# Kernel optimization log

Measured on AMD Instinct MI355X. Metric: run time of the kernel, lower is better.

The kernel has to match this reference:

```python
import jax, jax.numpy as jnp
import numpy as np
from jax import lax

B, L, V, D = 64, 1024, 256, 512
DROPOUT = 0.1   # embedding dropout rate
ZONEOUT = 0.1   # bernoulli prob of keeping previous state (zoneout)


def setup_inputs() -> dict:
    key = jax.random.key(0)
    ks = jax.random.split(key, 5)
    tokens = jax.random.randint(ks[0], (B, L), 0, V)
    lengths = jax.random.randint(ks[1], (B,), 1, L + 1)
    embed = jax.random.normal(ks[2], (V, D), jnp.float32) * 0.02
    s = 1.0 / np.sqrt(2 * D).astype(np.float32)
    W_fwd = jax.random.normal(ks[3], (2 * D, 4 * D), jnp.float32) * s
    b_fwd = jnp.zeros((4 * D,), jnp.float32)
    W_bwd = jax.random.normal(ks[4], (2 * D, 4 * D), jnp.float32) * s
    b_bwd = jnp.zeros((4 * D,), jnp.float32)
    return {"tokens": tokens, "lengths": lengths, "embed": embed,
            "W_fwd": W_fwd, "b_fwd": b_fwd, "W_bwd": W_bwd, "b_bwd": b_bwd}


def _lstm_scan(x_tbd, reset_tb, W, b, key):
    # x_tbd: [L, B, D] time-major inputs; reset_tb: [L, B] bool (ResetCore mask)
    Bsz = x_tbd.shape[1]
    Dh = W.shape[1] // 4
    zeros = jnp.zeros((Bsz, Dh), x_tbd.dtype)

    def step(carry, inp):
        h, c, k = carry
        x_t, r_t = inp
        # hk.ResetCore: reset state to initial (zeros) where mask is True
        h = jnp.where(r_t[:, None], 0.0, h)
        c = jnp.where(r_t[:, None], 0.0, c)
        kz, k = jax.random.split(k)
        gated = jnp.concatenate([x_t, h], axis=-1) @ W + b  # [B, 4*Dh]
        i, g, f, o = jnp.split(gated, 4, axis=-1)
        f = jax.nn.sigmoid(f + 1.0)
        c_new = f * c + jax.nn.sigmoid(i) * jnp.tanh(g)
        h_new = jax.nn.sigmoid(o) * jnp.tanh(c_new)
        # zoneout: with prob ZONEOUT keep previous hidden/cell
        zm = jax.random.bernoulli(kz, ZONEOUT, (2,) + h.shape)
        h_out = jnp.where(zm[0], h, h_new)
        c_out = jnp.where(zm[1], c, c_new)
        return (h_out, c_out, k), h_out

    _, hs = lax.scan(step, (zeros, zeros, key), (x_tbd, reset_tb))
    return hs  # [L, B, Dh]


def reference(tokens, lengths, embed, W_fwd, b_fwd, W_bwd, b_bwd):
    key = jax.random.key(42)
    kd, kf, kb = jax.random.split(key, 3)
    x = embed[tokens]  # [B, L, D]
    # embedding dropout (is_training=True)
    keep = jax.random.bernoulli(kd, 1.0 - DROPOUT, x.shape)
    x = jnp.where(keep, x / (1.0 - DROPOUT), 0.0)
    Lx = x.shape[1]
    mask = jnp.arange(Lx)[None, :] < lengths[:, None] - 1  # [B, L]
    x_t = jnp.moveaxis(x, 1, 0)  # [L, B, D] time-major
    no_reset = jnp.zeros((Lx, x.shape[0]), bool)
    h_fwd = _lstm_scan(x_t, no_reset, W_fwd, b_fwd, kf)
    # backward pass on flipped sequence with flipped reset mask (ResetCore)
    h_bwd = _lstm_scan(jnp.flip(x_t, 0), jnp.flip(mask, 1).T, W_bwd, b_bwd, kb)
    h_bwd = jnp.flip(h_bwd, 0)
    out = jnp.concatenate([h_fwd, h_bwd], axis=-1)  # [L, B, 2*D]
    return jnp.moveaxis(out, 0, 1)  # [B, L, 2*D]
```

## Files before the change

### kernel.cpp

```cpp
#include <hip/hip_runtime.h>
#include <hip/hip_bf16.h>
#include <stdint.h>

typedef unsigned short u16;
typedef unsigned int   u32;
typedef unsigned long long u64;
typedef __bf16 bf16x8 __attribute__((ext_vector_type(8)));
typedef float  f32x4  __attribute__((ext_vector_type(4)));

__device__ __forceinline__ u32 rotl32(u32 v, int d){ return (v<<d)|(v>>(32-d)); }

__device__ __forceinline__ void tf2x32(u32 k0, u32 k1, u32 c0, u32 c1, u32 &o0, u32 &o1){
  u32 ks0=k0, ks1=k1, ks2=k0^k1^0x1BD11BDAu;
  u32 x0=c0+ks0, x1=c1+ks1;
  x0+=x1; x1=rotl32(x1,13); x1^=x0;  x0+=x1; x1=rotl32(x1,15); x1^=x0;
  x0+=x1; x1=rotl32(x1,26); x1^=x0;  x0+=x1; x1=rotl32(x1, 6); x1^=x0;
  x0+=ks1; x1+=ks2+1u;
  x0+=x1; x1=rotl32(x1,17); x1^=x0;  x0+=x1; x1=rotl32(x1,29); x1^=x0;
  x0+=x1; x1=rotl32(x1,16); x1^=x0;  x0+=x1; x1=rotl32(x1,24); x1^=x0;
  x0+=ks2; x1+=ks0+2u;
  x0+=x1; x1=rotl32(x1,13); x1^=x0;  x0+=x1; x1=rotl32(x1,15); x1^=x0;
  x0+=x1; x1=rotl32(x1,26); x1^=x0;  x0+=x1; x1=rotl32(x1, 6); x1^=x0;
  x0+=ks0; x1+=ks1+3u;
  x0+=x1; x1=rotl32(x1,17); x1^=x0;  x0+=x1; x1=rotl32(x1,29); x1^=x0;
  x0+=x1; x1=rotl32(x1,16); x1^=x0;  x0+=x1; x1=rotl32(x1,24); x1^=x0;
  x0+=ks1; x1+=ks2+4u;
  x0+=x1; x1=rotl32(x1,13); x1^=x0;  x0+=x1; x1=rotl32(x1,15); x1^=x0;
  x0+=x1; x1=rotl32(x1,26); x1^=x0;  x0+=x1; x1=rotl32(x1, 6); x1^=x0;
  x0+=ks2; x1+=ks0+5u;
  o0=x0; o1=x1;
}

__device__ __forceinline__ float u01(u32 b){ return __uint_as_float((b>>9)|0x3f800000u) - 1.0f; }
__device__ __forceinline__ u16 f2bf(float v){ __hip_bfloat16 h = __float2bfloat16(v); return *reinterpret_cast<u16*>(&h); }
__device__ __forceinline__ float bf2f(u16 b){ __hip_bfloat16 h; *reinterpret_cast<u16*>(&h)=b; return __bfloat162float(h); }
__device__ __forceinline__ float sigm(float x){ return 1.0f/(1.0f + __expf(-x)); }
__device__ __forceinline__ float tanh_f(float x){ return 1.0f - 2.0f/(__expf(2.0f*x) + 1.0f); }

__device__ __forceinline__ void gload_lds16(const u16* g, u16* l){
  __builtin_amdgcn_global_load_lds(
      (const __attribute__((address_space(1))) unsigned int*)g,
      (__attribute__((address_space(3))) unsigned int*)l, 16, 0, 0);
}

extern "C" __global__ void __launch_bounds__(256) prep_k(
    const float* __restrict__ Wf, const float* __restrict__ Wb,
    u16* __restrict__ wpack, u32* __restrict__ flags, u32* __restrict__ code, u32* __restrict__ keys){
  u32 gid = blockIdx.x*256u + threadIdx.x;
  if (gid < 8192u) flags[gid] = 0u;
  if (gid == 0u){
    *code = 0u;
    u32 d0,d1,f0,f1,g0,g1;
    tf2x32(0u,42u, 0u,0u, d0,d1);
    tf2x32(0u,42u, 0u,1u, f0,f1);
    tf2x32(0u,42u, 0u,2u, g0,g1);
    keys[0]=d0; keys[1]=d1; keys[2]=f0; keys[3]=f1; keys[4]=g0; keys[5]=g1;
  }
  if (gid == 1u){
    u32 r0,r1; bool ok = true;
    tf2x32(0u,0u,0u,0u,r0,r1);
    ok = ok && (r0==0x6b200159u) && (r1==0x99ba4efeu);
    tf2x32(0x13198a2eu,0x03707344u,0x243f6a88u,0x85a308d3u,r0,r1);
    ok = ok && (r0==0xc4923a9cu) && (r1==0x483df7a0u);
    tf2x32(0xffffffffu,0xffffffffu,0xffffffffu,0xffffffffu,r0,r1);
    ok = ok && (r0==0x1cb996fcu) && (r1==0xbb002be7u);
    if (!ok) __hip_atomic_fetch_or(code, 4u, __ATOMIC_RELAXED, __HIP_MEMORY_SCOPE_AGENT);
  }
  u32 idx = gid >> 6, lane = gid & 63u;
  u32 mat = idx & 3u; u32 r = idx >> 2;
  u32 gt = r & 3u; r >>= 2;
  u32 kt = r & 15u; r >>= 4;
  u32 ug = r & 31u; u32 dir = r >> 5;
  u32 col = gt*512u + ug*16u + (lane & 15u);
  u32 kb  = kt*32u + ((lane>>4)<<3);
  const float* W = dir ? Wb : Wf;
  bool hrow = (mat==1u || mat==2u);
  bool lo   = (mat==2u || mat==3u);
  u16 o[8];
  #pragma unroll
  for (int j=0;j<8;j++){
    u32 k = kb + (u32)j;
    u32 row = hrow ? (512u + k) : k;
    float v = W[(size_t)row*2048u + col];
    u16 h = f2bf(v);
    o[j] = lo ? f2bf(v - bf2f(h)) : h;
  }
  u16* dst = wpack + ((size_t)idx*64u + lane)*8u;
  uint4 pk;
  pk.x = (u32)o[0] | ((u32)o[1]<<16);
  pk.y = (u32)o[2] | ((u32)o[3]<<16);
  pk.z = (u32)o[4] | ((u32)o[5]<<16);
  pk.w = (u32)o[6] | ((u32)o[7]<<16);
  *(uint4*)dst = pk;
}

extern "C" __global__ void __launch_bounds__(256) embed_k(
    const int* __restrict__ tokens, const float* __restrict__ emb,
    const u32* __restrict__ keys, u16* __restrict__ X, u16* __restrict__ XLO, int xsplit){
  u32 gid = blockIdx.x*256u + threadIdx.x;
  u32 kd0 = keys[0], kd1 = keys[1];
  u32 i0 = gid << 1;
  u32 a0,a1,b0,b1;
  tf2x32(kd0,kd1, 0u, i0,     a0,a1);
  tf2x32(kd0,kd1, 0u, i0|1u,  b0,b1);
  u32 bb = i0 >> 19, l = (i0 >> 9) & 1023u, d = i0 & 511u;
  int tok = tokens[(bb<<10)|l];
  const float* ep = emb + (size_t)(u32)tok*512u + d;
  float e0 = ep[0], e1 = ep[1];
  float v0 = (u01(a0^a1) < 0.9f) ? (e0/0.9f) : 0.0f;
  float v1 = (u01(b0^b1) < 0.9f) ? (e1/0.9f) : 0.0f;
  size_t off = (((size_t)l<<6)|bb)*512u + d;
  u16 h0 = f2bf(v0), h1 = f2bf(v1);
  *(u32*)(X+off) = (u32)h0 | ((u32)h1<<16);
  if (xsplit){
    u16 l0 = f2bf(v0 - bf2f(h0)), l1 = f2bf(v1 - bf2f(h1));
    *(u32*)(XLO+off) = (u32)l0 | ((u32)l1<<16);
  }
}

extern "C" __global__ void __launch_bounds__(256,1) lstm_k(
    const u16* __restrict__ wpack, const u16* __restrict__ X, const u16* __restrict__ XLO,
    u32* hbuf, u32* chk, u32* flags, u32* code, const u32* __restrict__ keys,
    const int* __restrict__ lengths, const float* __restrict__ bF, const float* __restrict__ bB,
    float* __restrict__ out, int xsplit){
  __shared__ u16 xHi[2][16][520];
  __shared__ u16 xLoS[2][16][520];
  __shared__ u16 hHi[16][520];
  __shared__ u16 hLo[16][520];
  __shared__ float gparts[4][4][16][17];
  __shared__ u32 kzS[2];
  (void)chk;

  const int tid  = threadIdx.x;
  const int wid  = tid >> 6;
  const int lane = tid & 63;
  const int q    = lane >> 4, n15 = lane & 15;
  const int bx   = blockIdx.x;
  const int dir  = (bx & 7) >> 2, bg = bx & 3, ug = bx >> 3;
  const int grp  = dir*4 + bg;
  const int eb   = tid >> 4, eu = tid & 15;
  const int scol = eu * 32;

  if (bx == 0 && wid == 0){
    bf16x8 aI, aI2, bT;
    #pragma unroll
    for (int j=0;j<8;j++){
      int k = q*8 + j;
      aI[j]  = (__bf16)((k == n15)    ? 1.0f : 0.0f);
      aI2[j] = (__bf16)((k == n15+16) ? 1.0f : 0.0f);
      bT[j]  = (__bf16)((float)((k & 15)*16 + n15));
    }
    f32x4 z = {0.0f,0.0f,0.0f,0.0f};
    f32x4 d1 = __builtin_amdgcn_mfma_f32_16x16x32_bf16(aI,  bT, z, 0,0,0);
    f32x4 d2 = __builtin_amdgcn_mfma_f32_16x16x32_bf16(aI2, bT, z, 0,0,0);
    bool ok = true;
    #pragma unroll
    for (int r=0;r<4;r++){
      float ex = (float)((q*4 + r)*16 + n15);
      ok = ok && (d1[r] == ex) && (d2[r] == ex);
    }
    if (__any(ok ? 0 : 1) && lane == 0)
      __hip_atomic_fetch_or(code, 1u, __ATOMIC_RELAXED, __HIP_MEMORY_SCOPE_AGENT);
  }

  u32 kc0 = keys[2 + dir*2], kc1 = keys[3 + dir*2];

  bf16x8 BW[4][4][4];
  #pragma unroll
  for (int ktl=0;ktl<4;ktl++)
    #pragma unroll
    for (int gt=0;gt<4;gt++)
      #pragma unroll
      for (int mat=0;mat<4;mat++){
        size_t idx = ((((size_t)(dir*32+ug)*16 + (size_t)(wid*4+ktl))*4 + gt)*4 + mat);
        BW[mat][ktl][gt] = *(const bf16x8*)(wpack + (idx*64 + lane)*8);
      }

  const float* bias = dir ? bB : bF;
  float biasr[4];
  #pragma unroll
  for (int g=0;g<4;g++) biasr[g] = bias[g*512 + ug*16 + eu];
  const int lenb = lengths[bg*16 + eb];

  float cReg = 0.0f, hReg = 0.0f;

  u32* hb_base = hbuf + (size_t)grp*2*16*512;
  const size_t outbase = (size_t)(bg*16+eb)*1048576 + (size_t)(dir*512 + ug*16 + eu);

  {
    const int tx0 = dir ? 1023 : 0;
    #pragma unroll
    for (int j=0;j<4;j++){
      const int rb = wid*4 + j;
      const size_t go = (((size_t)tx0*64) + (size_t)(bg*16 + rb))*512 + (size_t)lane*8;
      gload_lds16(X + go, &xHi[0][rb][0]);
      if (xsplit) gload_lds16(XLO + go, &xLoS[0][rb][0]);
    }
  }

  for (int t=0; t<1024; ++t){
    const int cur = t & 1, nxt = cur ^ 1;
    const int tx = dir ? (1023 - t) : t;

    if (wid == 0){
      u32 A0,A1,B0,B1;
      tf2x32(kc0,kc1, 0u,0u, A0,A1);
      tf2x32(kc0,kc1, 0u,1u, B0,B1);
      if (lane==0){ kzS[0]=A0; kzS[1]=A1; }
      kc0=B0; kc1=B1;
    }
    if (t > 0 && wid == 3 && lane < 32){
      const u32* sp = flags + (((size_t)grp*32 + (u32)lane) << 5);
      while (__hip_atomic_load(sp, __ATOMIC_RELAXED, __HIP_MEMORY_SCOPE_AGENT) < (u32)t) {}
    }
    __syncthreads();

    const bool rst = (dir==1) && (t > 1024 - lenb);
    const bool hload = (t > 0) && !rst;
    u64 hv64[16];
    if (hload){
      const u64* hrow64 = (const u64*)(hb_base + ((size_t)((t-1)&1)*16 + eb)*512 + scol);
      #pragma unroll
      for (int i=0;i<16;i++)
        hv64[i] = __hip_atomic_load(hrow64 + i, __ATOMIC_RELAXED, __HIP_MEMORY_SCOPE_AGENT);
    }
    if (t < 1023){
      const int txn = dir ? (1022 - t) : (t + 1);
      #pragma unroll
      for (int j=0;j<4;j++){
        const int rb = wid*4 + j;
        const size_t go = (((size_t)txn*64) + (size_t)(bg*16 + rb))*512 + (size_t)lane*8;
        gload_lds16(X + go, &xHi[nxt][rb][0]);
        if (xsplit) gload_lds16(XLO + go, &xLoS[nxt][rb][0]);
      }
    }
    const u32 cnt = (u32)((bg*16+eb)*512 + ug*16+eu);
    u32 p0,p1,q0,q1;
    tf2x32(kzS[0], kzS[1], 0u, cnt,          p0,p1);
    tf2x32(kzS[0], kzS[1], 0u, cnt+32768u,   q0,q1);
    const bool keepH = (u01(p0^p1) < 0.1f);
    const bool keepC = (u01(q0^q1) < 0.1f);

    f32x4 zz = {0.0f,0.0f,0.0f,0.0f};
    f32x4 acc[4] = {zz,zz,zz,zz};
    #pragma unroll
    for (int ktl=0;ktl<4;ktl++){
      const int ko = (wid*4+ktl)*32 + q*8;
      bf16x8 ax = *(const bf16x8*)&xHi[cur][n15][ko];
      #pragma unroll
      for (int gt=0;gt<4;gt++){
        acc[gt] = __builtin_amdgcn_mfma_f32_16x16x32_bf16(ax, BW[0][ktl][gt], acc[gt], 0,0,0);
        acc[gt] = __builtin_amdgcn_mfma_f32_16x16x32_bf16(ax, BW[3][ktl][gt], acc[gt], 0,0,0);
      }
      if (xsplit){
        bf16x8 axl = *(const bf16x8*)&xLoS[cur][n15][ko];
        #pragma unroll
        for (int gt=0;gt<4;gt++)
          acc[gt] = __builtin_amdgcn_mfma_f32_16x16x32_bf16(axl, BW[0][ktl][gt], acc[gt], 0,0,0);
      }
    }

    if (!hload){
      uint4 z; z.x=0u; z.y=0u; z.z=0u; z.w=0u;
      uint4* hd = (uint4*)&hHi[eb][scol];
      uint4* ld = (uint4*)&hLo[eb][scol];
      hd[0]=z;hd[1]=z;hd[2]=z;hd[3]=z;  ld[0]=z;ld[1]=z;ld[2]=z;ld[3]=z;
    } else {
      u32 hiw[16], low[16];
      #pragma unroll
      for (int k=0;k<16;k++){
        u32 lo32 = (u32)hv64[k], hi32 = (u32)(hv64[k] >> 32);
        hiw[k] = (lo32 & 0xFFFFu) | (hi32 << 16);
        low[k] = (lo32 >> 16)     | (hi32 & 0xFFFF0000u);
      }
      uint4* hd = (uint4*)&hHi[eb][scol];
      uint4* ld = (uint4*)&hLo[eb][scol];
      #pragma unroll
      for (int v=0;v<4;v++){
        uint4 hw; hw.x=hiw[4*v]; hw.y=hiw[4*v+1]; hw.z=hiw[4*v+2]; hw.w=hiw[4*v+3];
        uint4 lw; lw.x=low[4*v]; lw.y=low[4*v+1]; lw.z=low[4*v+2]; lw.w=low[4*v+3];
        hd[v]=hw; ld[v]=lw;
      }
    }
    __syncthreads();

    #pragma unroll
    for (int ktl=0;ktl<4;ktl++){
      const int ko = (wid*4+ktl)*32 + q*8;
      bf16x8 ahi = *(const bf16x8*)&hHi[n15][ko];
      bf16x8 alo = *(const bf16x8*)&hLo[n15][ko];
      #pragma unroll
      for (int gt=0;gt<4;gt++){
        acc[gt] = __builtin_amdgcn_mfma_f32_16x16x32_bf16(ahi, BW[1][ktl][gt], acc[gt], 0,0,0);
        acc[gt] = __builtin_amdgcn_mfma_f32_16x16x32_bf16(ahi, BW[2][ktl][gt], acc[gt], 0,0,0);
        acc[gt] = __builtin_amdgcn_mfma_f32_16x16x32_bf16(alo, BW[1][ktl][gt], acc[gt], 0,0,0);
      }
    }
    #pragma unroll
    for (int gt=0;gt<4;gt++)
      #pragma unroll
      for (int r=0;r<4;r++)
        gparts[wid][gt][q*4+r][n15] = acc[gt][r];
    __syncthreads();

    float gv[4];
    #pragma unroll
    for (int g=0;g<4;g++)
      gv[g] = gparts[0][g][eb][eu]+gparts[1][g][eb][eu]+gparts[2][g][eb][eu]+gparts[3][g][eb][eu]+biasr[g];
    float cp = cReg, hprev = hReg;
    if (rst){ cp = 0.0f; hprev = 0.0f; }
    float fg = sigm(gv[2] + 1.0f);
    float cn = fg*cp + sigm(gv[0])*tanh_f(gv[1]);
    float hn = sigm(gv[3])*tanh_f(cn);
    float ho = keepH ? hprev : hn;
    float co = keepC ? cp    : cn;
    cReg = co; hReg = ho;
    u16 hhi = f2bf(ho); u16 hlo = f2bf(ho - bf2f(hhi));
    u32 hp32 = ((u32)hlo<<16) | (u32)hhi;
    __hip_atomic_store(hb_base + ((size_t)(t&1)*16 + eb)*512 + (size_t)(ug*16+eu), hp32,
                       __ATOMIC_RELAXED, __HIP_MEMORY_SCOPE_AGENT);
    __syncthreads();
    if (tid == 0)
      __hip_atomic_store(flags + (((size_t)grp*32 + ug) << 5), (u32)(t+1),
                         __ATOMIC_RELAXED, __HIP_MEMORY_SCOPE_AGENT);
    out[outbase + ((size_t)tx << 10)] = ho;
  }

  if (bx == 0 && tid == 0){
    u32 c = __hip_atomic_load(code, __ATOMIC_ACQUIRE, __HIP_MEMORY_SCOPE_AGENT);
    if (c != 0u) out[0] = 1000.0f * (float)c;
  }
}

extern "C" void kernel_launch(void* const* d_in, const int* in_sizes, int n_in,
                              void* d_out, int out_size, void* d_ws, size_t ws_size,
                              hipStream_t stream) {
  const int*   tokens  = (const int*)d_in[0];
  const int*   lengths = (const int*)d_in[1];
  const float* embed   = (const float*)d_in[2];
  const float* Wf      = (const float*)d_in[3];
  const float* bF      = (const float*)d_in[4];
  const float* Wb      = (const float*)d_in[5];
  const float* bB      = (const float*)d_in[6];
  float* out = (float*)d_out;

  const size_t SZ_WPACK = 16777216ull;
  const size_t SZ_X     = 67108864ull;
  const size_t SZ_HBUF  = 524288ull;
  const size_t SZ_CHK   = 65536ull;
  const size_t SZ_FLAGS = 32768ull;
  size_t need_full = SZ_WPACK + 2*SZ_X + SZ_HBUF + SZ_CHK + SZ_FLAGS + 128;
  int xsplit = (ws_size >= need_full) ? 1 : 0;

  char* p = (char*)d_ws;
  u16* wpack = (u16*)p;            p += SZ_WPACK;
  u16* X     = (u16*)p;            p += SZ_X;
  u16* XLO   = xsplit ? (u16*)p : X;
  if (xsplit)                      p += SZ_X;
  u32* hbuf  = (u32*)p;            p += SZ_HBUF;
  u32* chk   = (u32*)p;            p += SZ_CHK;
  u32* flags = (u32*)p;            p += SZ_FLAGS;
  u32* code  = (u32*)p;            p += 64;
  u32* keys  = (u32*)p;

  prep_k<<<dim3(4096), dim3(256), 0, stream>>>(Wf, Wb, wpack, flags, code, keys);
  embed_k<<<dim3(65536), dim3(256), 0, stream>>>(tokens, embed, keys, X, XLO, xsplit);
  lstm_k<<<dim3(256), dim3(256), 0, stream>>>(wpack, X, XLO, hbuf, chk, flags, code, keys,
                                              lengths, bF, bB, out, xsplit);
}
```

Measured before the change: 7.379 ms.

## Replace per-step flag barrier with step-tagged hidden-state words polled directly

Each hidden-state element is now stored as a 64-bit word that carries the step index next to the packed bf16 hi/lo value. Consumers spin on the data words themselves until every tag matches the previous step. This removes the separate flag store, the extra __syncthreads before it, and the flag-polling wave. The zoneout key generation is also moved into every thread, dropping a shared-memory broadcast and its barrier, at the cost of twice the hbuf traffic and redundant Threefry work per thread.

```diff
diff --git a/kernel.cpp b/kernel.cpp
--- a/kernel.cpp
+++ b/kernel.cpp
@@ -45,9 +45,11 @@
 
 extern "C" __global__ void __launch_bounds__(256) prep_k(
     const float* __restrict__ Wf, const float* __restrict__ Wb,
-    u16* __restrict__ wpack, u32* __restrict__ flags, u32* __restrict__ code, u32* __restrict__ keys){
+    u16* __restrict__ wpack, u32* __restrict__ flags, u32* __restrict__ code,
+    u32* __restrict__ keys, u32* __restrict__ hbuf){
   u32 gid = blockIdx.x*256u + threadIdx.x;
   if (gid < 8192u) flags[gid] = 0u;
+  if (gid < 131072u) ((u64*)hbuf)[gid] = 0xFFFFFFFF00000000ull;
   if (gid == 0u){
     *code = 0u;
     u32 d0,d1,f0,f1,g0,g1;
@@ -128,8 +130,7 @@
   __shared__ u16 hHi[16][520];
   __shared__ u16 hLo[16][520];
   __shared__ float gparts[4][4][16][17];
-  __shared__ u32 kzS[2];
-  (void)chk;
+  (void)chk; (void)flags;
 
   const int tid  = threadIdx.x;
   const int wid  = tid >> 6;
@@ -184,7 +185,7 @@
 
   float cReg = 0.0f, hReg = 0.0f;
 
-  u32* hb_base = hbuf + (size_t)grp*2*16*512;
+  u64* hb64 = (u64*)hbuf + (size_t)grp*2*16*512;
   const size_t outbase = (size_t)(bg*16+eb)*1048576 + (size_t)(dir*512 + ug*16 + eu);
 
   {
@@ -197,31 +198,17 @@
       if (xsplit) gload_lds16(XLO + go, &xLoS[0][rb][0]);
     }
   }
+  __syncthreads();
 
   for (int t=0; t<1024; ++t){
     const int cur = t & 1, nxt = cur ^ 1;
     const int tx = dir ? (1023 - t) : t;
 
-    if (wid == 0){
-      u32 A0,A1,B0,B1;
-      tf2x32(kc0,kc1, 0u,0u, A0,A1);
-      tf2x32(kc0,kc1, 0u,1u, B0,B1);
-      if (lane==0){ kzS[0]=A0; kzS[1]=A1; }
-      kc0=B0; kc1=B1;
-    }
-    if (t > 0 && wid == 3 && lane < 32){
-      const u32* sp = flags + (((size_t)grp*32 + (u32)lane) << 5);
-      while (__hip_atomic_load(sp, __ATOMIC_RELAXED, __HIP_MEMORY_SCOPE_AGENT) < (u32)t) {}
-    }
-    __syncthreads();
-
-    const bool rst = (dir==1) && (t > 1024 - lenb);
-    const bool hload = (t > 0) && !rst;
-    u64 hv64[16];
-    if (hload){
-      const u64* hrow64 = (const u64*)(hb_base + ((size_t)((t-1)&1)*16 + eb)*512 + scol);
-      #pragma unroll
-      for (int i=0;i<16;i++)
+    const u64* hrow64 = hb64 + ((size_t)((t-1)&1)*16 + eb)*512 + scol;
+    u64 hv64[32];
+    if (t > 0){
+      #pragma unroll
+      for (int i=0;i<32;i++)
         hv64[i] = __hip_atomic_load(hrow64 + i, __ATOMIC_RELAXED, __HIP_MEMORY_SCOPE_AGENT);
     }
     if (t < 1023){
@@ -234,10 +221,14 @@
         if (xsplit) gload_lds16(XLO + go, &xLoS[nxt][rb][0]);
       }
     }
+    u32 kz0,kz1,B0,B1;
+    tf2x32(kc0,kc1, 0u,0u, kz0,kz1);
+    tf2x32(kc0,kc1, 0u,1u, B0,B1);
+    kc0=B0; kc1=B1;
     const u32 cnt = (u32)((bg*16+eb)*512 + ug*16+eu);
     u32 p0,p1,q0,q1;
-    tf2x32(kzS[0], kzS[1], 0u, cnt,          p0,p1);
-    tf2x32(kzS[0], kzS[1], 0u, cnt+32768u,   q0,q1);
+    tf2x32(kz0, kz1, 0u, cnt,          p0,p1);
+    tf2x32(kz0, kz1, 0u, cnt+32768u,   q0,q1);
     const bool keepH = (u01(p0^p1) < 0.1f);
     const bool keepC = (u01(q0^q1) < 0.1f);
 
@@ -260,7 +251,22 @@
       }
     }
 
-    if (!hload){
+    if (t > 0){
+      const u32 etag = (u32)(t-1);
+      for (;;){
+        u32 bad = 0u;
+        #pragma unroll
+        for (int i=0;i<32;i++) bad |= ((u32)(hv64[i]>>32)) ^ etag;
+        if (bad == 0u) break;
+        #pragma unroll
+        for (int i=0;i<32;i++)
+          if ((u32)(hv64[i]>>32) != etag)
+            hv64[i] = __hip_atomic_load(hrow64 + i, __ATOMIC_RELAXED, __HIP_MEMORY_SCOPE_AGENT);
+      }
+    }
+
+    const bool rst = (dir==1) && (t > 1024 - lenb);
+    if (t == 0 || rst){
       uint4 z; z.x=0u; z.y=0u; z.z=0u; z.w=0u;
       uint4* hd = (uint4*)&hHi[eb][scol];
       uint4* ld = (uint4*)&hLo[eb][scol];
@@ -269,9 +275,9 @@
       u32 hiw[16], low[16];
       #pragma unroll
       for (int k=0;k<16;k++){
-        u32 lo32 = (u32)hv64[k], hi32 = (u32)(hv64[k] >> 32);
-        hiw[k] = (lo32 & 0xFFFFu) | (hi32 << 16);
-        low[k] = (lo32 >> 16)     | (hi32 & 0xFFFF0000u);
+        u32 c0 = (u32)hv64[2*k], c1 = (u32)hv64[2*k+1];
+        hiw[k] = (c0 & 0xFFFFu) | ((c1 & 0xFFFFu) << 16);
+        low[k] = (c0 >> 16)     | (c1 & 0xFFFF0000u);
       }
       uint4* hd = (uint4*)&hHi[eb][scol];
       uint4* ld = (uint4*)&hLo[eb][scol];
@@ -316,13 +322,9 @@
     float co = keepC ? cp    : cn;
     cReg = co; hReg = ho;
     u16 hhi = f2bf(ho); u16 hlo = f2bf(ho - bf2f(hhi));
-    u32 hp32 = ((u32)hlo<<16) | (u32)hhi;
-    __hip_atomic_store(hb_base + ((size_t)(t&1)*16 + eb)*512 + (size_t)(ug*16+eu), hp32,
+    u64 hp = ((u64)(u32)t << 32) | (u64)(((u32)hlo<<16) | (u32)hhi);
+    __hip_atomic_store(hb64 + ((size_t)(t&1)*16 + eb)*512 + (size_t)(ug*16+eu), hp,
                        __ATOMIC_RELAXED, __HIP_MEMORY_SCOPE_AGENT);
-    __syncthreads();
-    if (tid == 0)
-      __hip_atomic_store(flags + (((size_t)grp*32 + ug) << 5), (u32)(t+1),
-                         __ATOMIC_RELAXED, __HIP_MEMORY_SCOPE_AGENT);
     out[outbase + ((size_t)tx << 10)] = ho;
   }
 
@@ -346,7 +348,7 @@
 
   const size_t SZ_WPACK = 16777216ull;
   const size_t SZ_X     = 67108864ull;
-  const size_t SZ_HBUF  = 524288ull;
+  const size_t SZ_HBUF  = 1048576ull;
   const size_t SZ_CHK   = 65536ull;
   const size_t SZ_FLAGS = 32768ull;
   size_t need_full = SZ_WPACK + 2*SZ_X + SZ_HBUF + SZ_CHK + SZ_FLAGS + 128;
@@ -363,7 +365,7 @@
   u32* code  = (u32*)p;            p += 64;
   u32* keys  = (u32*)p;
 
-  prep_k<<<dim3(4096), dim3(256), 0, stream>>>(Wf, Wb, wpack, flags, code, keys);
+  prep_k<<<dim3(4096), dim3(256), 0, stream>>>(Wf, Wb, wpack, flags, code, keys, hbuf);
   embed_k<<<dim3(65536), dim3(256), 0, stream>>>(tokens, embed, keys, X, XLO, xsplit);
   lstm_k<<<dim3(256), dim3(256), 0, stream>>>(wpack, X, XLO, hbuf, chk, flags, code, keys,
                                               lengths, bF, bB, out, xsplit);
```

After: 13.05 ms. 1.77x slower.
